# Kernel tuning notes

Hardware: AMD Instinct MI355X
Metric: run time of the kernel (lower is better)

Reference implementation:

```python
import jax, jax.numpy as jnp
import numpy as np

HIDDEN = 128
N_RBF = 32
LMAX = 2
N_NODES = 10000
DEG = 8  # each node has DEG outgoing (and DEG incoming) edges on a ring


def _build_graph():
    src = np.repeat(np.arange(N_NODES, dtype=np.int64), DEG)
    offs = np.tile(np.arange(1, DEG + 1, dtype=np.int64), N_NODES)
    dst = (src + offs) % N_NODES
    keys = src * N_NODES + dst
    order = np.argsort(keys)
    src2, dst2 = src[order], dst[order]  # e2 sorted by key (searchsorted invariant)
    e1_to_e2 = np.empty_like(order)
    e1_to_e2[order] = np.arange(order.size)
    return src, dst, src2, dst2, e1_to_e2


def setup_inputs() -> dict:
    key = jax.random.key(0)
    ks = jax.random.split(key, 12)
    src1, dst1, src2, dst2, e1_to_e2 = _build_graph()
    E1, E2 = src1.size, src2.size
    in_dim = 6 * HIDDEN + 3 * N_RBF + 1  # 865

    def lin(k, fi, fo):
        kw, kb = jax.random.split(k)
        s = 1.0 / np.sqrt(fi)
        return (jax.random.uniform(kw, (fi, fo), minval=-s, maxval=s),
                jax.random.uniform(kb, (fo,), minval=-s, maxval=s))

    w1, b1 = lin(ks[0], in_dim, HIDDEN)
    w2, b2 = lin(ks[1], HIDDEN, HIDDEN)
    wgw, bgw = lin(ks[2], HIDDEN, HIDDEN)
    wgt, bgt = lin(ks[3], HIDDEN, HIDDEN)
    return {
        "t_e2": jax.random.normal(ks[4], (E2, HIDDEN), dtype=jnp.float32),
        "h": jax.random.normal(ks[5], (N_NODES, HIDDEN), dtype=jnp.float32),
        "edge_index1": jnp.asarray(np.stack([src1, dst1])),
        "edge_index2": jnp.asarray(np.stack([src2, dst2])),
        "e1_to_e2": jnp.asarray(e1_to_e2),
        "dist_e1": jax.random.uniform(ks[6], (E1,), dtype=jnp.float32),
        "dist_e2": jax.random.uniform(ks[7], (E2,), dtype=jnp.float32),
        "rbf_e1": jax.random.normal(ks[8], (E1, N_RBF), dtype=jnp.float32),
        "rbf_e2": jax.random.normal(ks[9], (E2, N_RBF), dtype=jnp.float32),
        "sph_e1": jax.random.normal(ks[10], (E1, LMAX + 1), dtype=jnp.float32),
        "num_nodes": N_NODES,
        "w1": w1, "b1": b1, "w2": w2, "b2": b2,
        "wgw": wgw, "bgw": bgw, "wgt": wgt, "bgt": bgt,
    }


def _wedge_indices(edge_index1, edge_index2, num_nodes):
    """Host-side (numpy, vectorized) wedge construction: for every center node k,
    all (incoming edge i->k, outgoing edge k->j) pairs with i != j, kept only when
    (i, j) itself is an edge in e2 (looked up by sorted key search)."""
    src1 = np.asarray(edge_index1[0]); dst1 = np.asarray(edge_index1[1])
    src2 = np.asarray(edge_index2[0]); dst2 = np.asarray(edge_index2[1])
    nz = src1 != dst1  # drop self-loops
    s, d = src1[nz], dst1[nz]
    eid = np.nonzero(nz)[0]
    out_deg = np.bincount(s, minlength=num_nodes)
    out_order = np.argsort(s, kind="stable")  # filtered-edge positions grouped by src
    out_ptr = np.concatenate([np.zeros(1, np.int64), np.cumsum(out_deg)])
    reps = out_deg[d]  # each incoming edge pairs with out_deg[center] outgoing edges
    total = int(reps.sum())
    if total == 0:
        z = np.zeros(0, np.int64)
        return z, z, z, z, z, z
    starts = np.cumsum(reps) - reps
    local = np.arange(total) - np.repeat(starts, reps)
    kj_f = out_order[np.repeat(out_ptr[d], reps) + local]
    i = np.repeat(s, reps)
    k = np.repeat(d, reps)
    eik = np.repeat(eid, reps)
    j = d[kj_f]
    ekj = eid[kj_f]
    m = i != j
    i, k, j, eik, ekj = i[m], k[m], j[m], eik[m], ekj[m]
    e2_keys = src2.astype(np.int64) * num_nodes + dst2
    pk = i.astype(np.int64) * num_nodes + j
    pos = np.searchsorted(e2_keys, pk)
    posc = np.minimum(pos, e2_keys.size - 1)
    valid = (pos < e2_keys.size) & (e2_keys[posc] == pk)
    return i[valid], k[valid], j[valid], eik[valid], ekj[valid], posc[valid]


def reference(t_e2, h, edge_index1, edge_index2, e1_to_e2, dist_e1, dist_e2,
              rbf_e1, rbf_e2, sph_e1, num_nodes,
              w1, b1, w2, b2, wgw, bgw, wgt, bgt):
    i, k, j, eik, ekj, eij = _wedge_indices(edge_index1, edge_index2, int(num_nodes))
    if i.size == 0:
        return t_e2
    i, k, j = jnp.asarray(i), jnp.asarray(k), jnp.asarray(j)
    eik, ekj, eij = jnp.asarray(eik), jnp.asarray(ekj), jnp.asarray(eij)
    e1e2 = jnp.asarray(e1_to_e2)
    # wedge geometric features (wedge_use_high_degree=False -> l=1 contraction only)
    c_feat = (sph_e1[eik, 1] * sph_e1[ekj, 1])[:, None]           # [W, 1]
    g = jnp.concatenate([rbf_e1[eik], rbf_e1[ekj], rbf_e2[eij], c_feat], axis=-1)
    rho_in = jnp.concatenate([t_e2[e1e2[eik]], t_e2[e1e2[ekj]], t_e2[eij],
                              h[i], h[k], h[j], g], axis=-1)       # [W, 865]
    msg = jax.nn.silu(rho_in @ w1 + b1) @ w2 + b2                  # [W, H]
    m = jax.ops.segment_sum(msg, eij, num_segments=t_e2.shape[0])  # [E2, H]
    return t_e2 + jax.nn.sigmoid(m @ wgw + bgw) * jnp.tanh(t_e2 @ wgt + bgt)
```

## Files before the change

### kernel.cpp

```cpp
#include <hip/hip_runtime.h>
#include <math.h>

typedef unsigned short u16;
typedef unsigned int u32;
typedef __bf16 bf16x8 __attribute__((ext_vector_type(8)));
typedef float f32x4 __attribute__((ext_vector_type(4)));

__device__ __forceinline__ float bf2f(u16 v){ union{u32 u;float f;}c; c.u=((u32)v)<<16; return c.f; }
__device__ __forceinline__ u16 f2bf(float f){ union{__bf16 h; u16 u;}c; c.h=(__bf16)f; return c.u; }
__device__ __forceinline__ u32 pk2(float a, float b){
  union{ __bf16 h[2]; u32 u; }c; c.h[0]=(__bf16)a; c.h[1]=(__bf16)b; return c.u;
}
__device__ __forceinline__ uint4 ld8f(const float* p){
  float4 x = ((const float4*)p)[0];
  float4 y = ((const float4*)p)[1];
  uint4 r; r.x=pk2(x.x,x.y); r.y=pk2(x.z,x.w); r.z=pk2(y.x,y.y); r.w=pk2(y.z,y.w);
  return r;
}
__device__ __forceinline__ float fsilu(float x){ return x/(1.f+__expf(-x)); }

__global__ void k_setup_all(const int* __restrict__ e1_to_e2,
                            const float* __restrict__ rbf_e1,
                            const float* __restrict__ sph_e1,
                            u16* __restrict__ rbf1p, float* __restrict__ sph_c, int E1,
                            const int* __restrict__ src2, int* __restrict__ out_ptr,
                            int Nn, int E2,
                            const float* __restrict__ w1, u16* __restrict__ WbigT,
                            const float* __restrict__ w2, const float* __restrict__ wgw,
                            const float* __restrict__ wgt, const float* __restrict__ b2,
                            u16* __restrict__ WcT, u16* __restrict__ WgtT,
                            float* __restrict__ bc2, int* __restrict__ cnt,
                            int nb0, int nb1, int nb2, int nb3) {
  const int b = blockIdx.x, t = threadIdx.x;
  if (b < nb0) {
    int e = b*256 + t;
    if (e >= E1) return;
    int f = e1_to_e2[e];
    sph_c[f] = sph_e1[e*3+1];
    const float* s = rbf_e1 + (size_t)e*32;
    uint4* d = (uint4*)(rbf1p + (size_t)f*32);
    d[0]=ld8f(s); d[1]=ld8f(s+8); d[2]=ld8f(s+16); d[3]=ld8f(s+24);
  } else if (b < nb1) {
    int n = (b-nb0)*256 + t;
    if (n > Nn) return;
    int lo=0, hi=E2;
    while (lo<hi){ int m=(lo+hi)>>1; if (src2[m]<n) lo=m+1; else hi=m; }
    out_ptr[n]=lo;
  } else if (b < nb2) {
    int id = (b-nb1)*256 + t;
    if (id >= 384*448) return;
    int n = id/448, k = id%448;
    int q = n>>7, nn = n&127;
    int row = -1;
    if (k<128) row = q*128+k;
    else if (k<256) { if (q==0) row = 384+(k-128); }
    else if (k<384) { if (q==0) row = 512+(k-256); else if (q==1) row = 640+(k-256); }
    else if (k<416) { if (q==0) row = 768+(k-384); else if (q==1) row = 800+(k-384); }
    else { if (q==2) row = 832+(k-416); }
    WbigT[id] = (row>=0) ? f2bf(w1[row*128+nn]) : (u16)0;
  } else if (b < nb3) {
    int id = (b-nb2)*256 + t;
    if (id < 16384) {
      int n = id&127, k = id>>7;
      float s = 0.f;
      for (int r=0;r<128;r++) s += w2[k*128+r]*wgw[r*128+n];
      WcT[n*128+k] = f2bf(s);
      WgtT[n*128+k] = f2bf(wgt[k*128+n]);
    } else if (id < 16384+128) {
      int n = id-16384;
      float s = 0.f;
      for (int r=0;r<128;r++) s += b2[r]*wgw[r*128+n];
      bc2[n] = s;
    }
  } else {
    int i = (b-nb3)*256 + t;
    if (i < E2) cnt[i] = 0;
  }
}

__global__ __launch_bounds__(256, 8)
void k_enum(const int* __restrict__ src2, const int* __restrict__ dst2,
            const int* __restrict__ out_ptr, const float* __restrict__ sph_c,
            int4* __restrict__ wrec, int* __restrict__ cnt, int E2) {
  int id = blockIdx.x*256 + threadIdx.x;
  if (id >= E2*8) return;
  int gw = id >> 3, d = id & 7;
  int i = src2[gw], j = dst2[gw];
  int f = out_ptr[i] + d;
  if (f >= out_ptr[i+1]) return;
  int k = dst2[f];
  int lo = out_ptr[k], hi = out_ptr[k+1], hi0 = hi;
  while (lo<hi) { int m=(lo+hi)>>1; if (dst2[m]<j) lo=m+1; else hi=m; }
  if (lo < hi0 && dst2[lo]==j) {
    float cf = sph_c[f]*sph_c[lo];
    int slot = atomicAdd(&cnt[gw], 1);
    int4 r; r.x=f; r.y=lo; r.z=__float_as_int(cf); r.w=0;
    wrec[(size_t)gw*8 + slot] = r;
  }
}

__global__ __launch_bounds__(256, 8)
void k_wedge2(const u16* __restrict__ Q1, const u16* __restrict__ Q2,
              const u16* __restrict__ P3, const int4* __restrict__ wrec,
              const int* __restrict__ cnt, const float* __restrict__ w1,
              u16* __restrict__ S, int E2) {
  int gw = (int)((blockIdx.x*256 + threadIdx.x) >> 6);
  int lane = threadIdx.x & 63;
  if (gw >= E2) return;
  u32 p3u = ((const u32*)(P3 + (size_t)gw*128))[lane];
  float p30 = bf2f((u16)(p3u&0xffff)), p31 = bf2f((u16)(p3u>>16));
  float2 wv = ((const float2*)(w1 + 864*128))[lane];
  const u32* q1b = (const u32*)Q1;
  const u32* q2b = (const u32*)Q2;
  const int4* wr = wrec + (size_t)gw*8;
  int c = cnt[gw];
  float a0=0.f, a1=0.f;
  int w = 0;
  for (; w+2<=c; w+=2) {
    int4 rA = wr[w], rB = wr[w+1];
    u32 xA = q1b[(size_t)rA.x*64 + lane];
    u32 yA = q2b[(size_t)rA.y*64 + lane];
    u32 xB = q1b[(size_t)rB.x*64 + lane];
    u32 yB = q2b[(size_t)rB.y*64 + lane];
    float cfA = __int_as_float(rA.z), cfB = __int_as_float(rB.z);
    float x0 = p30 + bf2f((u16)(xA&0xffff)) + bf2f((u16)(yA&0xffff)) + cfA*wv.x;
    float x1 = p31 + bf2f((u16)(xA>>16))    + bf2f((u16)(yA>>16))    + cfA*wv.y;
    float z0 = p30 + bf2f((u16)(xB&0xffff)) + bf2f((u16)(yB&0xffff)) + cfB*wv.x;
    float z1 = p31 + bf2f((u16)(xB>>16))    + bf2f((u16)(yB>>16))    + cfB*wv.y;
    a0 += fsilu(x0) + fsilu(z0);
    a1 += fsilu(x1) + fsilu(z1);
  }
  if (w < c) {
    int4 rA = wr[w];
    u32 xA = q1b[(size_t)rA.x*64 + lane];
    u32 yA = q2b[(size_t)rA.y*64 + lane];
    float cfA = __int_as_float(rA.z);
    float x0 = p30 + bf2f((u16)(xA&0xffff)) + bf2f((u16)(yA&0xffff)) + cfA*wv.x;
    float x1 = p31 + bf2f((u16)(xA>>16))    + bf2f((u16)(yA>>16))    + cfA*wv.y;
    a0 += fsilu(x0);
    a1 += fsilu(x1);
  }
  ((u32*)(S + (size_t)gw*128))[lane] = pk2(a0, a1);
}

struct GArgs {
  const float* t_f32; const float* h; const float* rbf_e2;
  const u16* rbf1p; const u16* Asrc;
  const int* src2; const int* dst2; const int* cnt;
  const u16* Bmat; const u16* Bmat2;
  const float* b1; const float* bgw; const float* bgt; const float* bc2;
  u16* out0; u16* out1; u16* out2;
  float* outf;
  int M;
};

__global__ __launch_bounds__(256, 2)
void k_gemm0(GArgs a) {
  const int nwg = gridDim.x;
  const int id  = blockIdx.x;
  const int xcd = id & 7, idx = id >> 3;
  const int q = nwg >> 3, r = nwg & 7;
  const int w = (xcd < r ? xcd*(q+1) : r*(q+1) + (xcd-r)*q) + idx;
  const int bm = w/3, bn = w - bm*3;

  constexpr int KT = 448;
  constexpr int NK = KT/32;
  __shared__ u16 As[128*40];
  __shared__ u16 Bs[128*40];
  const int tid = threadIdx.x;
  const int lane = tid & 63, wave = tid >> 6;
  const int wm = wave >> 1, wn = wave & 1;
  const int quad = lane >> 4, l16 = lane & 15;

  const int part = tid & 3;
  const int ra = tid >> 2;
  const int rb = ra + 64;
  long fa = (long)bm*128 + ra;
  long fb = (long)bm*128 + rb;
  if (fa >= a.M) fa = a.M-1;
  if (fb >= a.M) fb = a.M-1;
  const int sa=a.src2[fa], da=a.dst2[fa], sb=a.src2[fb], db=a.dst2[fb];

  f32x4 acc[4][4] = {};
  for (int ks=0; ks<NK; ks++) {
    const int kb = ks*32;
    uint4 va, vb;
    if (ks<4)       { va = ld8f(a.t_f32 + fa*128 + kb + part*8);
                      vb = ld8f(a.t_f32 + fb*128 + kb + part*8); }
    else if (ks<8)  { va = ld8f(a.h + (long)sa*128 + (kb-128) + part*8);
                      vb = ld8f(a.h + (long)sb*128 + (kb-128) + part*8); }
    else if (ks<12) { va = ld8f(a.h + (long)da*128 + (kb-256) + part*8);
                      vb = ld8f(a.h + (long)db*128 + (kb-256) + part*8); }
    else if (ks==12){ va = *(const uint4*)(a.rbf1p + fa*32 + part*8);
                      vb = *(const uint4*)(a.rbf1p + fb*32 + part*8); }
    else            { va = ld8f(a.rbf_e2 + fa*32 + part*8);
                      vb = ld8f(a.rbf_e2 + fb*32 + part*8); }
    uint4 wa = *(const uint4*)(a.Bmat + (long)(bn*128 + ra)*KT + kb + part*8);
    uint4 wb = *(const uint4*)(a.Bmat + (long)(bn*128 + rb)*KT + kb + part*8);
    __syncthreads();
    *(uint4*)(As + ra*40 + part*8) = va;
    *(uint4*)(As + rb*40 + part*8) = vb;
    *(uint4*)(Bs + ra*40 + part*8) = wa;
    *(uint4*)(Bs + rb*40 + part*8) = wb;
    __syncthreads();
    bf16x8 af[4], bfr[4];
    #pragma unroll
    for (int t=0;t<4;t++) {
      af[t]  = *(const bf16x8*)(As + (wm*64 + t*16 + l16)*40 + quad*8);
      bfr[t] = *(const bf16x8*)(Bs + (wn*64 + t*16 + l16)*40 + quad*8);
    }
    #pragma unroll
    for (int tm=0;tm<4;tm++)
      #pragma unroll
      for (int tn=0;tn<4;tn++)
        acc[tm][tn] = __builtin_amdgcn_mfma_f32_16x16x32_bf16(af[tm], bfr[tn], acc[tm][tn], 0,0,0);
  }

  #pragma unroll
  for (int tm=0;tm<4;tm++) {
    const int rloc = wm*64 + tm*16 + quad*4;
    #pragma unroll
    for (int r=0;r<4;r++) {
      long row = (long)bm*128 + rloc + r;
      if (row >= a.M) continue;
      #pragma unroll
      for (int tn=0;tn<4;tn++) {
        const int col = wn*64 + tn*16 + l16;
        float v = acc[tm][tn][r];
        u16* dst = (bn==0)? a.out0 : (bn==1)? a.out1 : a.out2;
        if (bn==2) v += a.b1[col];
        dst[row*128 + col] = f2bf(v);
      }
    }
  }
}

__global__ __launch_bounds__(256, 2)
void k_gemm12(GArgs a) {
  __shared__ u16 As[128*40];
  __shared__ u16 Bs[128*40];
  const int tid = threadIdx.x;
  const int bm = blockIdx.x;
  const int lane = tid & 63, wave = tid >> 6;
  const int wm = wave >> 1, wn = wave & 1;
  const int quad = lane >> 4, l16 = lane & 15;

  const int part = tid & 3;
  const int ra = tid >> 2;
  const int rb = ra + 64;
  long fa = (long)bm*128 + ra;
  long fb = (long)bm*128 + rb;
  if (fa >= a.M) fa = a.M-1;
  if (fb >= a.M) fb = a.M-1;

  f32x4 acc1[4][4] = {};
  f32x4 acc2[4][4] = {};
  for (int ks=0; ks<4; ks++) {
    const int kb = ks*32;
    uint4 va = *(const uint4*)(a.Asrc + fa*128 + kb + part*8);
    uint4 vb = *(const uint4*)(a.Asrc + fb*128 + kb + part*8);
    uint4 wa = *(const uint4*)(a.Bmat + (long)ra*128 + kb + part*8);
    uint4 wbv= *(const uint4*)(a.Bmat + (long)rb*128 + kb + part*8);
    __syncthreads();
    *(uint4*)(As + ra*40 + part*8) = va;
    *(uint4*)(As + rb*40 + part*8) = vb;
    *(uint4*)(Bs + ra*40 + part*8) = wa;
    *(uint4*)(Bs + rb*40 + part*8) = wbv;
    __syncthreads();
    bf16x8 af[4], bfr[4];
    #pragma unroll
    for (int t=0;t<4;t++) {
      af[t]  = *(const bf16x8*)(As + (wm*64 + t*16 + l16)*40 + quad*8);
      bfr[t] = *(const bf16x8*)(Bs + (wn*64 + t*16 + l16)*40 + quad*8);
    }
    #pragma unroll
    for (int tm=0;tm<4;tm++)
      #pragma unroll
      for (int tn=0;tn<4;tn++)
        acc1[tm][tn] = __builtin_amdgcn_mfma_f32_16x16x32_bf16(af[tm], bfr[tn], acc1[tm][tn], 0,0,0);
  }
  for (int ks=0; ks<4; ks++) {
    const int kb = ks*32;
    uint4 va = ld8f(a.t_f32 + fa*128 + kb + part*8);
    uint4 vb = ld8f(a.t_f32 + fb*128 + kb + part*8);
    uint4 wa = *(const uint4*)(a.Bmat2 + (long)ra*128 + kb + part*8);
    uint4 wbv= *(const uint4*)(a.Bmat2 + (long)rb*128 + kb + part*8);
    __syncthreads();
    *(uint4*)(As + ra*40 + part*8) = va;
    *(uint4*)(As + rb*40 + part*8) = vb;
    *(uint4*)(Bs + ra*40 + part*8) = wa;
    *(uint4*)(Bs + rb*40 + part*8) = wbv;
    __syncthreads();
    bf16x8 af[4], bfr[4];
    #pragma unroll
    for (int t=0;t<4;t++) {
      af[t]  = *(const bf16x8*)(As + (wm*64 + t*16 + l16)*40 + quad*8);
      bfr[t] = *(const bf16x8*)(Bs + (wn*64 + t*16 + l16)*40 + quad*8);
    }
    #pragma unroll
    for (int tm=0;tm<4;tm++)
      #pragma unroll
      for (int tn=0;tn<4;tn++)
        acc2[tm][tn] = __builtin_amdgcn_mfma_f32_16x16x32_bf16(af[tm], bfr[tn], acc2[tm][tn], 0,0,0);
  }

  #pragma unroll
  for (int tm=0;tm<4;tm++) {
    const int rloc = wm*64 + tm*16 + quad*4;
    #pragma unroll
    for (int r=0;r<4;r++) {
      long row = (long)bm*128 + rloc + r;
      if (row >= a.M) continue;
      #pragma unroll
      for (int tn=0;tn<4;tn++) {
        const int col = wn*64 + tn*16 + l16;
        float u = acc1[tm][tn][r] + (float)a.cnt[row]*a.bc2[col] + a.bgw[col];
        float g = 1.f/(1.f+__expf(-u));
        float vv = acc2[tm][tn][r] + a.bgt[col];
        float th = 1.f - 2.f/(__expf(2.f*vv)+1.f);
        float t  = a.t_f32[row*128+col];
        a.outf[row*128+col] = t + g*th;
      }
    }
  }
}

extern "C" void kernel_launch(void* const* d_in, const int* in_sizes, int n_in,
                              void* d_out, int out_size, void* d_ws, size_t ws_size,
                              hipStream_t stream) {
  const float* t_e2  = (const float*)d_in[0];
  const float* h     = (const float*)d_in[1];
  const int* ei2     = (const int*)d_in[3];
  const int* e1_to_e2 = (const int*)d_in[4];
  const float* rbf_e1 = (const float*)d_in[7];
  const float* rbf_e2 = (const float*)d_in[8];
  const float* sph_e1 = (const float*)d_in[9];
  const float* w1  = (const float*)d_in[11];
  const float* b1  = (const float*)d_in[12];
  const float* w2  = (const float*)d_in[13];
  const float* b2  = (const float*)d_in[14];
  const float* wgw = (const float*)d_in[15];
  const float* bgw = (const float*)d_in[16];
  const float* wgt = (const float*)d_in[17];
  const float* bgt = (const float*)d_in[18];

  const int E2 = in_sizes[0]/128;
  const int Nn = in_sizes[1]/128;
  const int E1 = in_sizes[5];
  const int* src2 = ei2;
  const int* dst2 = ei2 + E2;

  char* p = (char*)d_ws;
  u16* Q1 = (u16*)p;       p += (size_t)E2*128*2;
  u16* Q2 = (u16*)p;       p += (size_t)E2*128*2;
  u16* P3 = (u16*)p;       p += (size_t)E2*128*2;
  u16* rbf1p = (u16*)p;    p += (size_t)E2*32*2;
  u16* WbigT = (u16*)p;    p += (size_t)384*448*2;
  u16* WcT   = (u16*)p;    p += (size_t)128*128*2;
  u16* WgtT  = (u16*)p;    p += (size_t)128*128*2;
  float* sph_c = (float*)p; p += (size_t)E2*4;
  float* bc2   = (float*)p; p += 512;
  int* out_ptr = (int*)p;   p += (((size_t)(Nn+1)*4 + 63)/64)*64;
  int* cnt     = (int*)p;   p += (size_t)E2*4;
  int4* wrec   = (int4*)p;  p += (size_t)E2*8*16;
  u16* S = P3;

  const int nb_edges = (E1+255)/256;
  const int nb_ptr   = (Nn+1+255)/256;
  const int nb_wbig  = (384*448+255)/256;
  const int nb_small = (16512+255)/256;
  const int nb_cnt   = (E2+255)/256;
  const int nb0 = nb_edges;
  const int nb1 = nb0 + nb_ptr;
  const int nb2 = nb1 + nb_wbig;
  const int nb3 = nb2 + nb_small;
  const int nbT = nb3 + nb_cnt;
  k_setup_all<<<nbT, 256, 0, stream>>>(e1_to_e2, rbf_e1, sph_e1, rbf1p, sph_c, E1,
                                       src2, out_ptr, Nn, E2,
                                       w1, WbigT, w2, wgw, wgt, b2,
                                       WcT, WgtT, bc2, cnt,
                                       nb0, nb1, nb2, nb3);
  k_enum<<<(E2*8+255)/256, 256, 0, stream>>>(src2, dst2, out_ptr, sph_c, wrec, cnt, E2);

  const int Mb = (E2+127)/128;
  {
    GArgs a = {};
    a.t_f32=t_e2; a.h=h; a.rbf1p=rbf1p; a.rbf_e2=rbf_e2;
    a.src2=src2; a.dst2=dst2; a.Bmat=WbigT; a.b1=b1;
    a.out0=Q1; a.out1=Q2; a.out2=P3; a.M=E2;
    k_gemm0<<<Mb*3, 256, 0, stream>>>(a);
  }
  k_wedge2<<<(E2+3)/4, 256, 0, stream>>>(Q1, Q2, P3, wrec, cnt, w1, S, E2);
  {
    GArgs a = {};
    a.Asrc=S; a.cnt=cnt; a.Bmat=WcT; a.Bmat2=WgtT;
    a.bgw=bgw; a.bgt=bgt; a.bc2=bc2; a.t_f32=t_e2;
    a.outf=(float*)d_out; a.M=E2;
    k_gemm12<<<Mb, 256, 0, stream>>>(a);
  }
}
```

Measured before the change: 329.5 us.

## Drop zero blocks from first-layer GEMM and fuse wedge enumeration into wedge kernel

The first-layer weight matrix is split into three per-output-block matrices with K of 416, 288 and 160, so each column block of k_gemm0 only iterates over its nonzero K slices instead of a padded 448. The separate wedge-enumeration kernel and its wedge record buffer are removed. Each wedge warp now finds valid wedges itself with 8 lanes, compacts them via ballot and shuffles, and writes the count. This saves a kernel launch, the record round trip through memory and the cnt zeroing, but gives k_gemm0 uneven per-block work and puts the binary search latency inside the wedge kernel.

```diff
diff --git a/kernel.cpp b/kernel.cpp
--- a/kernel.cpp
+++ b/kernel.cpp
@@ -25,12 +25,14 @@
                             u16* __restrict__ rbf1p, float* __restrict__ sph_c, int E1,
                             const int* __restrict__ src2, int* __restrict__ out_ptr,
                             int Nn, int E2,
-                            const float* __restrict__ w1, u16* __restrict__ WbigT,
+                            const float* __restrict__ w1,
+                            u16* __restrict__ W0T, u16* __restrict__ W1T,
+                            u16* __restrict__ W2T,
                             const float* __restrict__ w2, const float* __restrict__ wgw,
                             const float* __restrict__ wgt, const float* __restrict__ b2,
                             u16* __restrict__ WcT, u16* __restrict__ WgtT,
-                            float* __restrict__ bc2, int* __restrict__ cnt,
-                            int nb0, int nb1, int nb2, int nb3) {
+                            float* __restrict__ bc2,
+                            int nb0, int nb1, int nb2) {
   const int b = blockIdx.x, t = threadIdx.x;
   if (b < nb0) {
     int e = b*256 + t;
@@ -48,17 +50,22 @@
     out_ptr[n]=lo;
   } else if (b < nb2) {
     int id = (b-nb1)*256 + t;
-    if (id >= 384*448) return;
-    int n = id/448, k = id%448;
-    int q = n>>7, nn = n&127;
-    int row = -1;
-    if (k<128) row = q*128+k;
-    else if (k<256) { if (q==0) row = 384+(k-128); }
-    else if (k<384) { if (q==0) row = 512+(k-256); else if (q==1) row = 640+(k-256); }
-    else if (k<416) { if (q==0) row = 768+(k-384); else if (q==1) row = 800+(k-384); }
-    else { if (q==2) row = 832+(k-416); }
-    WbigT[id] = (row>=0) ? f2bf(w1[row*128+nn]) : (u16)0;
-  } else if (b < nb3) {
+    if (id < 128*416) {
+      int n = id/416, k = id - n*416;
+      int row = (k<128)? k : (k<256)? 384+(k-128) : (k<384)? 512+(k-256) : 768+(k-384);
+      W0T[id] = f2bf(w1[row*128+n]);
+    } else if (id < 128*(416+288)) {
+      int id2 = id - 128*416;
+      int n = id2/288, k = id2 - n*288;
+      int row = (k<128)? 128+k : (k<256)? 640+(k-128) : 800+(k-256);
+      W1T[id2] = f2bf(w1[row*128+n]);
+    } else if (id < 128*864) {
+      int id2 = id - 128*704;
+      int n = id2/160, k = id2 - n*160;
+      int row = (k<128)? 256+k : 832+(k-128);
+      W2T[id2] = f2bf(w1[row*128+n]);
+    }
+  } else {
     int id = (b-nb2)*256 + t;
     if (id < 16384) {
       int n = id&127, k = id>>7;
@@ -72,73 +79,58 @@
       for (int r=0;r<128;r++) s += b2[r]*wgw[r*128+n];
       bc2[n] = s;
     }
-  } else {
-    int i = (b-nb3)*256 + t;
-    if (i < E2) cnt[i] = 0;
   }
 }
 
 __global__ __launch_bounds__(256, 8)
-void k_enum(const int* __restrict__ src2, const int* __restrict__ dst2,
-            const int* __restrict__ out_ptr, const float* __restrict__ sph_c,
-            int4* __restrict__ wrec, int* __restrict__ cnt, int E2) {
-  int id = blockIdx.x*256 + threadIdx.x;
-  if (id >= E2*8) return;
-  int gw = id >> 3, d = id & 7;
-  int i = src2[gw], j = dst2[gw];
-  int f = out_ptr[i] + d;
-  if (f >= out_ptr[i+1]) return;
-  int k = dst2[f];
-  int lo = out_ptr[k], hi = out_ptr[k+1], hi0 = hi;
-  while (lo<hi) { int m=(lo+hi)>>1; if (dst2[m]<j) lo=m+1; else hi=m; }
-  if (lo < hi0 && dst2[lo]==j) {
-    float cf = sph_c[f]*sph_c[lo];
-    int slot = atomicAdd(&cnt[gw], 1);
-    int4 r; r.x=f; r.y=lo; r.z=__float_as_int(cf); r.w=0;
-    wrec[(size_t)gw*8 + slot] = r;
-  }
-}
-
-__global__ __launch_bounds__(256, 8)
-void k_wedge2(const u16* __restrict__ Q1, const u16* __restrict__ Q2,
-              const u16* __restrict__ P3, const int4* __restrict__ wrec,
-              const int* __restrict__ cnt, const float* __restrict__ w1,
-              u16* __restrict__ S, int E2) {
+void k_wedge(const int* __restrict__ src2, const int* __restrict__ dst2,
+             const int* __restrict__ out_ptr, const float* __restrict__ sph_c,
+             const u16* __restrict__ Q1, const u16* __restrict__ Q2,
+             const u16* __restrict__ P3, const float* __restrict__ w1,
+             u16* __restrict__ S, int* __restrict__ cnt, int E2) {
   int gw = (int)((blockIdx.x*256 + threadIdx.x) >> 6);
   int lane = threadIdx.x & 63;
   if (gw >= E2) return;
+  int i = src2[gw], j = dst2[gw];
+  int f = 0, lo = 0; float cf = 0.f; bool valid = false;
+  if (lane < 8) {
+    int ff = out_ptr[i] + lane;
+    if (ff < out_ptr[i+1]) {
+      int k = dst2[ff];
+      int l = out_ptr[k], hh = out_ptr[k+1], h0 = hh;
+      while (l<hh){ int m=(l+hh)>>1; if (dst2[m]<j) l=m+1; else hh=m; }
+      if (l<h0 && dst2[l]==j){ valid=true; f=ff; lo=l; cf=sph_c[ff]*sph_c[l]; }
+    }
+  }
+  unsigned long long mask = __ballot(valid);
+  if (lane==0) cnt[gw] = __popcll(mask);
   u32 p3u = ((const u32*)(P3 + (size_t)gw*128))[lane];
   float p30 = bf2f((u16)(p3u&0xffff)), p31 = bf2f((u16)(p3u>>16));
   float2 wv = ((const float2*)(w1 + 864*128))[lane];
   const u32* q1b = (const u32*)Q1;
   const u32* q2b = (const u32*)Q2;
-  const int4* wr = wrec + (size_t)gw*8;
-  int c = cnt[gw];
   float a0=0.f, a1=0.f;
-  int w = 0;
-  for (; w+2<=c; w+=2) {
-    int4 rA = wr[w], rB = wr[w+1];
-    u32 xA = q1b[(size_t)rA.x*64 + lane];
-    u32 yA = q2b[(size_t)rA.y*64 + lane];
-    u32 xB = q1b[(size_t)rB.x*64 + lane];
-    u32 yB = q2b[(size_t)rB.y*64 + lane];
-    float cfA = __int_as_float(rA.z), cfB = __int_as_float(rB.z);
-    float x0 = p30 + bf2f((u16)(xA&0xffff)) + bf2f((u16)(yA&0xffff)) + cfA*wv.x;
-    float x1 = p31 + bf2f((u16)(xA>>16))    + bf2f((u16)(yA>>16))    + cfA*wv.y;
-    float z0 = p30 + bf2f((u16)(xB&0xffff)) + bf2f((u16)(yB&0xffff)) + cfB*wv.x;
-    float z1 = p31 + bf2f((u16)(xB>>16))    + bf2f((u16)(yB>>16))    + cfB*wv.y;
-    a0 += fsilu(x0) + fsilu(z0);
-    a1 += fsilu(x1) + fsilu(z1);
-  }
-  if (w < c) {
-    int4 rA = wr[w];
-    u32 xA = q1b[(size_t)rA.x*64 + lane];
-    u32 yA = q2b[(size_t)rA.y*64 + lane];
-    float cfA = __int_as_float(rA.z);
-    float x0 = p30 + bf2f((u16)(xA&0xffff)) + bf2f((u16)(yA&0xffff)) + cfA*wv.x;
-    float x1 = p31 + bf2f((u16)(xA>>16))    + bf2f((u16)(yA>>16))    + cfA*wv.y;
-    a0 += fsilu(x0);
-    a1 += fsilu(x1);
+  while (mask) {
+    int bA = __ffsll(mask)-1; mask &= mask-1;
+    int fA = __shfl(f,bA), lA = __shfl(lo,bA); float cA = __shfl(cf,bA);
+    if (mask) {
+      int bB = __ffsll(mask)-1; mask &= mask-1;
+      int fB = __shfl(f,bB), lB = __shfl(lo,bB); float cB = __shfl(cf,bB);
+      u32 xA = q1b[(size_t)fA*64+lane], yA = q2b[(size_t)lA*64+lane];
+      u32 xB = q1b[(size_t)fB*64+lane], yB = q2b[(size_t)lB*64+lane];
+      float x0 = p30 + bf2f((u16)(xA&0xffff)) + bf2f((u16)(yA&0xffff)) + cA*wv.x;
+      float x1 = p31 + bf2f((u16)(xA>>16))    + bf2f((u16)(yA>>16))    + cA*wv.y;
+      float z0 = p30 + bf2f((u16)(xB&0xffff)) + bf2f((u16)(yB&0xffff)) + cB*wv.x;
+      float z1 = p31 + bf2f((u16)(xB>>16))    + bf2f((u16)(yB>>16))    + cB*wv.y;
+      a0 += fsilu(x0) + fsilu(z0);
+      a1 += fsilu(x1) + fsilu(z1);
+    } else {
+      u32 xA = q1b[(size_t)fA*64+lane], yA = q2b[(size_t)lA*64+lane];
+      float x0 = p30 + bf2f((u16)(xA&0xffff)) + bf2f((u16)(yA&0xffff)) + cA*wv.x;
+      float x1 = p31 + bf2f((u16)(xA>>16))    + bf2f((u16)(yA>>16))    + cA*wv.y;
+      a0 += fsilu(x0);
+      a1 += fsilu(x1);
+    }
   }
   ((u32*)(S + (size_t)gw*128))[lane] = pk2(a0, a1);
 }
@@ -147,6 +139,7 @@
   const float* t_f32; const float* h; const float* rbf_e2;
   const u16* rbf1p; const u16* Asrc;
   const int* src2; const int* dst2; const int* cnt;
+  const u16* B0; const u16* B1; const u16* B2;
   const u16* Bmat; const u16* Bmat2;
   const float* b1; const float* bgw; const float* bgt; const float* bc2;
   u16* out0; u16* out1; u16* out2;
@@ -163,8 +156,6 @@
   const int w = (xcd < r ? xcd*(q+1) : r*(q+1) + (xcd-r)*q) + idx;
   const int bm = w/3, bn = w - bm*3;
 
-  constexpr int KT = 448;
-  constexpr int NK = KT/32;
   __shared__ u16 As[128*40];
   __shared__ u16 Bs[128*40];
   const int tid = threadIdx.x;
@@ -179,24 +170,32 @@
   long fb = (long)bm*128 + rb;
   if (fa >= a.M) fa = a.M-1;
   if (fb >= a.M) fb = a.M-1;
-  const int sa=a.src2[fa], da=a.dst2[fa], sb=a.src2[fb], db=a.dst2[fb];
+  int sa=0, sb=0, da=0, db=0;
+  if (bn==0) { sa=a.src2[fa]; sb=a.src2[fb]; }
+  if (bn<2)  { da=a.dst2[fa]; db=a.dst2[fb]; }
+
+  const u16* Bp = (bn==0)? a.B0 : (bn==1)? a.B1 : a.B2;
+  const int NK = (bn==0)? 13 : (bn==1)? 9 : 5;
+  const int KT = NK*32;
 
   f32x4 acc[4][4] = {};
   for (int ks=0; ks<NK; ks++) {
     const int kb = ks*32;
     uint4 va, vb;
-    if (ks<4)       { va = ld8f(a.t_f32 + fa*128 + kb + part*8);
-                      vb = ld8f(a.t_f32 + fb*128 + kb + part*8); }
-    else if (ks<8)  { va = ld8f(a.h + (long)sa*128 + (kb-128) + part*8);
-                      vb = ld8f(a.h + (long)sb*128 + (kb-128) + part*8); }
-    else if (ks<12) { va = ld8f(a.h + (long)da*128 + (kb-256) + part*8);
-                      vb = ld8f(a.h + (long)db*128 + (kb-256) + part*8); }
-    else if (ks==12){ va = *(const uint4*)(a.rbf1p + fa*32 + part*8);
-                      vb = *(const uint4*)(a.rbf1p + fb*32 + part*8); }
-    else            { va = ld8f(a.rbf_e2 + fa*32 + part*8);
-                      vb = ld8f(a.rbf_e2 + fb*32 + part*8); }
-    uint4 wa = *(const uint4*)(a.Bmat + (long)(bn*128 + ra)*KT + kb + part*8);
-    uint4 wb = *(const uint4*)(a.Bmat + (long)(bn*128 + rb)*KT + kb + part*8);
+    if (ks<4)                    { va = ld8f(a.t_f32 + fa*128 + kb + part*8);
+                                   vb = ld8f(a.t_f32 + fb*128 + kb + part*8); }
+    else if (bn==0 && ks<8)      { va = ld8f(a.h + (long)sa*128 + (kb-128) + part*8);
+                                   vb = ld8f(a.h + (long)sb*128 + (kb-128) + part*8); }
+    else if (bn==0 && ks<12)     { va = ld8f(a.h + (long)da*128 + (kb-256) + part*8);
+                                   vb = ld8f(a.h + (long)db*128 + (kb-256) + part*8); }
+    else if (bn==1 && ks<8)      { va = ld8f(a.h + (long)da*128 + (kb-128) + part*8);
+                                   vb = ld8f(a.h + (long)db*128 + (kb-128) + part*8); }
+    else if (bn==2)              { va = ld8f(a.rbf_e2 + fa*32 + part*8);
+                                   vb = ld8f(a.rbf_e2 + fb*32 + part*8); }
+    else                         { va = *(const uint4*)(a.rbf1p + fa*32 + part*8);
+                                   vb = *(const uint4*)(a.rbf1p + fb*32 + part*8); }
+    uint4 wa = *(const uint4*)(Bp + (long)ra*KT + kb + part*8);
+    uint4 wb = *(const uint4*)(Bp + (long)rb*KT + kb + part*8);
     __syncthreads();
     *(uint4*)(As + ra*40 + part*8) = va;
     *(uint4*)(As + rb*40 + part*8) = vb;
@@ -355,42 +354,43 @@
   u16* Q2 = (u16*)p;       p += (size_t)E2*128*2;
   u16* P3 = (u16*)p;       p += (size_t)E2*128*2;
   u16* rbf1p = (u16*)p;    p += (size_t)E2*32*2;
-  u16* WbigT = (u16*)p;    p += (size_t)384*448*2;
+  u16* W0T = (u16*)p;      p += (size_t)128*416*2;
+  u16* W1T = (u16*)p;      p += (size_t)128*288*2;
+  u16* W2T = (u16*)p;      p += (size_t)128*160*2;
   u16* WcT   = (u16*)p;    p += (size_t)128*128*2;
   u16* WgtT  = (u16*)p;    p += (size_t)128*128*2;
   float* sph_c = (float*)p; p += (size_t)E2*4;
   float* bc2   = (float*)p; p += 512;
   int* out_ptr = (int*)p;   p += (((size_t)(Nn+1)*4 + 63)/64)*64;
   int* cnt     = (int*)p;   p += (size_t)E2*4;
-  int4* wrec   = (int4*)p;  p += (size_t)E2*8*16;
   u16* S = P3;
 
   const int nb_edges = (E1+255)/256;
   const int nb_ptr   = (Nn+1+255)/256;
-  const int nb_wbig  = (384*448+255)/256;
+  const int nb_w     = (128*864+255)/256;
   const int nb_small = (16512+255)/256;
-  const int nb_cnt   = (E2+255)/256;
   const int nb0 = nb_edges;
   const int nb1 = nb0 + nb_ptr;
-  const int nb2 = nb1 + nb_wbig;
-  const int nb3 = nb2 + nb_small;
-  const int nbT = nb3 + nb_cnt;
+  const int nb2 = nb1 + nb_w;
+  const int nbT = nb2 + nb_small;
   k_setup_all<<<nbT, 256, 0, stream>>>(e1_to_e2, rbf_e1, sph_e1, rbf1p, sph_c, E1,
                                        src2, out_ptr, Nn, E2,
-                                       w1, WbigT, w2, wgw, wgt, b2,
-                                       WcT, WgtT, bc2, cnt,
-                                       nb0, nb1, nb2, nb3);
-  k_enum<<<(E2*8+255)/256, 256, 0, stream>>>(src2, dst2, out_ptr, sph_c, wrec, cnt, E2);
+                                       w1, W0T, W1T, W2T,
+                                       w2, wgw, wgt, b2,
+                                       WcT, WgtT, bc2,
+                                       nb0, nb1, nb2);
 
   const int Mb = (E2+127)/128;
   {
     GArgs a = {};
     a.t_f32=t_e2; a.h=h; a.rbf1p=rbf1p; a.rbf_e2=rbf_e2;
-    a.src2=src2; a.dst2=dst2; a.Bmat=WbigT; a.b1=b1;
+    a.src2=src2; a.dst2=dst2;
+    a.B0=W0T; a.B1=W1T; a.B2=W2T; a.b1=b1;
     a.out0=Q1; a.out1=Q2; a.out2=P3; a.M=E2;
     k_gemm0<<<Mb*3, 256, 0, stream>>>(a);
   }
-  k_wedge2<<<(E2+3)/4, 256, 0, stream>>>(Q1, Q2, P3, wrec, cnt, w1, S, E2);
+  k_wedge<<<(E2+3)/4, 256, 0, stream>>>(src2, dst2, out_ptr, sph_c,
+                                        Q1, Q2, P3, w1, S, cnt, E2);
   {
     GArgs a = {};
     a.Asrc=S; a.cnt=cnt; a.Bmat=WcT; a.Bmat2=WgtT;
```

Measured after the change: 295.0 us. -10.5%, faster.
